# Performance work log

Hardware: AMD Instinct MI355X
Metric: run time of the kernel (lower is better)

## Reference

```python
import jax, jax.numpy as jnp
import numpy as np

# dims: batch, tokens, model dim, heads, head_dim, context len, n_blocks, ffn dim
B, L, D, H, HD, S, NB, DFF = 1, 3072, 1024, 16, 64, 512, 2, 4096
T3, H3, W3 = 12, 16, 16  # latent video grid, T3*H3*W3 == L


def _ln(x):
    # LayerNorm, elementwise_affine=False, eps=1e-6
    m = jnp.mean(x, axis=-1, keepdims=True)
    v = jnp.mean(jnp.square(x - m), axis=-1, keepdims=True)
    return (x - m) * jax.lax.rsqrt(v + 1e-6)


def _rot_half(x):
    x1, x2 = jnp.split(x, 2, axis=-1)
    return jnp.concatenate([-x2, x1], axis=-1)


def _rope3d(head_dim, t, h, w):
    d = head_dim // 6
    def band(n):
        freqs = 1.0 / 10000.0 ** (np.arange(0, 2 * d, 2, dtype=np.float32) / (2 * d))
        return np.outer(np.arange(n, dtype=np.float32), freqs)  # [n, d]
    te, he, we = band(t), band(h), band(w)
    rope = np.zeros((t, h, w, head_dim), dtype=np.float32)
    rope[:, :, :, :d] = te[:, None, None, :]
    rope[:, :, :, d:2 * d] = he[None, :, None, :]
    rope[:, :, :, 2 * d:3 * d] = we[None, None, :, :]
    return jnp.asarray(rope.reshape(t * h * w, head_dim))


def _forward(x, timestep_emb, context_emb, rope_emb, adaW, adab, sqW, skW, svW,
             soW, sob, cqW, ckW, cvW, coW, cob, f1W, f1b, f2W, f2b):
    Bv, Lv, Dv = x.shape
    hd = rope_emb.shape[-1]
    nh = Dv // hd
    scale = hd ** -0.5
    cos = jnp.cos(rope_emb)[None, None]  # [1,1,L,hd]
    sin = jnp.sin(rope_emb)[None, None]

    def heads(y):  # [B,N,D] -> [B,H,N,hd]
        return y.reshape(Bv, -1, nh, hd).transpose(0, 2, 1, 3)

    def merge(y):  # [B,H,L,hd] -> [B,L,D]
        return y.transpose(0, 2, 1, 3).reshape(Bv, Lv, Dv)

    for i in range(adaW.shape[0]):
        mods = timestep_emb @ adaW[i].T + adab[i]  # [B, 6D]
        sh_msa, sc_msa, g_msa, sh_mlp, sc_mlp, g_mlp = jnp.split(mods, 6, axis=-1)
        # --- AdaLN + self-attention with RoPE ---
        hx = _ln(x) * (1.0 + sc_msa[:, None, :]) + sh_msa[:, None, :]
        q, k, v = heads(hx @ sqW[i].T), heads(hx @ skW[i].T), heads(hx @ svW[i].T)
        q = q * cos + _rot_half(q) * sin
        k = k * cos + _rot_half(k) * sin
        a = jax.nn.softmax(jnp.einsum('bhld,bhmd->bhlm', q, k) * scale, axis=-1)
        o = merge(jnp.einsum('bhlm,bhmd->bhld', a, v))
        x = x + g_msa[:, None, :] * (o @ soW[i].T + sob[i])
        # --- cross-attention (no gate, no modulation) ---
        hx = _ln(x)
        q = heads(hx @ cqW[i].T)
        k = heads(context_emb @ ckW[i].T)
        v = heads(context_emb @ cvW[i].T)
        a = jax.nn.softmax(jnp.einsum('bhld,bhsd->bhls', q, k) * scale, axis=-1)
        o = merge(jnp.einsum('bhls,bhsd->bhld', a, v))
        x = x + (o @ coW[i].T + cob[i])
        # --- AdaLN + MLP (exact GELU) ---
        hx = _ln(x) * (1.0 + sc_mlp[:, None, :]) + sh_mlp[:, None, :]
        hx = jax.nn.gelu(hx @ f1W[i].T + f1b[i], approximate=False)
        x = x + g_mlp[:, None, :] * (hx @ f2W[i].T + f2b[i])
    return x


def setup_inputs() -> dict:
    ks = jax.random.split(jax.random.key(0), 20)
    s = 0.02
    return {
        'x': jax.random.normal(ks[0], (B, L, D), jnp.float32),
        'timestep_emb': jax.random.normal(ks[1], (B, D), jnp.float32),
        'context_emb': jax.random.normal(ks[2], (B, S, D), jnp.float32),
        'rope_emb': _rope3d(HD, T3, H3, W3),
        'adaW': jax.random.normal(ks[3], (NB, 6 * D, D), jnp.float32) * s,
        'adab': jnp.zeros((NB, 6 * D), jnp.float32),
        'sqW': jax.random.normal(ks[4], (NB, D, D), jnp.float32) * s,
        'skW': jax.random.normal(ks[5], (NB, D, D), jnp.float32) * s,
        'svW': jax.random.normal(ks[6], (NB, D, D), jnp.float32) * s,
        'soW': jax.random.normal(ks[7], (NB, D, D), jnp.float32) * s,
        'sob': jnp.zeros((NB, D), jnp.float32),
        'cqW': jax.random.normal(ks[8], (NB, D, D), jnp.float32) * s,
        'ckW': jax.random.normal(ks[9], (NB, D, D), jnp.float32) * s,
        'cvW': jax.random.normal(ks[10], (NB, D, D), jnp.float32) * s,
        'coW': jax.random.normal(ks[11], (NB, D, D), jnp.float32) * s,
        'cob': jnp.zeros((NB, D), jnp.float32),
        'f1W': jax.random.normal(ks[12], (NB, DFF, D), jnp.float32) * s,
        'f1b': jnp.zeros((NB, DFF), jnp.float32),
        'f2W': jax.random.normal(ks[13], (NB, D, DFF), jnp.float32) * s,
        'f2b': jnp.zeros((NB, D), jnp.float32),
    }


def reference(x, timestep_emb, context_emb, rope_emb, adaW, adab, sqW, skW, svW,
              soW, sob, cqW, ckW, cvW, coW, cob, f1W, f1b, f2W, f2b):
    return _forward(x, timestep_emb, context_emb, rope_emb, adaW, adab, sqW, skW,
                    svW, soW, sob, cqW, ckW, cvW, coW, cob, f1W, f1b, f2W, f2b)
```

## Files before the change

### kernel.cpp

```cpp
#include <hip/hip_runtime.h>
#include <math.h>

typedef __attribute__((ext_vector_type(8))) short bf16x8;
typedef __attribute__((ext_vector_type(4))) float f32x4;
typedef unsigned short u16;
typedef unsigned int u32;

#define DEV static __device__ __forceinline__

typedef __attribute__((address_space(3))) u32 lds_u32;
typedef const __attribute__((address_space(1))) u32 glb_u32;

DEV void gload16(const void* g, void* l){
  __builtin_amdgcn_global_load_lds((glb_u32*)g, (lds_u32*)l, 16, 0, 0);
}

DEV u16 f2bf(float f){
  u32 u = __builtin_bit_cast(u32, f);
  u32 r = (u + 0x7fffu + ((u >> 16) & 1u)) >> 16;
  return (u16)r;
}
DEV float bf2f(u16 h){
  u32 u = ((u32)h) << 16;
  return __builtin_bit_cast(float, u);
}
DEV u32 cvtpk(float a, float b){
  u32 r;
  asm("v_cvt_pk_bf16_f32 %0, %1, %2" : "=v"(r) : "v"(a), "v"(b));
  return r;
}
DEV float gelu_exact(float x){ return 0.5f*x*(1.f+erff(x*0.70710678118654752f)); }

#define QSCALE 0.18033688f

DEV void xcd_remap(int &bx, int &by){
  int gx = gridDim.x, gy = gridDim.y;
  int n = gx*gy;
  if ((n & 7) == 0){
    int id = by*gx + bx;
    int q = n >> 3;
    int sid = (id & 7)*q + (id >> 3);
    bx = sid % gx;
    by = sid / gx;
  }
}

__global__ __launch_bounds__(256) void k_copy_f32(const float* __restrict__ in, float* __restrict__ out, int n4){
  int i = blockIdx.x*256 + threadIdx.x;
  if (i < n4) ((float4*)out)[i] = ((const float4*)in)[i];
}

__global__ __launch_bounds__(256) void k_cvt_bf16(const float* __restrict__ in, u16* __restrict__ out, int n4){
  int i = blockIdx.x*256 + threadIdx.x;
  if (i < n4){
    float4 v = ((const float4*)in)[i];
    ushort4 o;
    o.x = f2bf(v.x); o.y = f2bf(v.y); o.z = f2bf(v.z); o.w = f2bf(v.w);
    ((ushort4*)out)[i] = o;
  }
}

struct CvtArgs { const float4* s[16]; ushort4* d[16]; };
__global__ __launch_bounds__(256) void k_cvt_all(CvtArgs a){
  int i = blockIdx.x*256 + threadIdx.x;
  int seg = i >> 19;
  int off = i & 0x7FFFF;
  float4 v = a.s[seg][off];
  ushort4 o;
  o.x = f2bf(v.x); o.y = f2bf(v.y); o.z = f2bf(v.z); o.w = f2bf(v.w);
  a.d[seg][off] = o;
}

__global__ __launch_bounds__(256) void k_trig(const float* __restrict__ rope,
    float2* __restrict__ ctq, float2* __restrict__ ctk){
  int i = blockIdx.x*256 + threadIdx.x;
  int d = i & 63;
  float a = rope[i];
  float c = cosf(a), s = sinf(a);
  float sg = (d < 32) ? -s : s;
  ctk[i] = make_float2(c, sg);
  ctq[i] = make_float2(c*QSCALE, sg*QSCALE);
}

__global__ __launch_bounds__(256) void k_ada(const float* __restrict__ te,
    const float* __restrict__ adaW, const float* __restrict__ adab,
    float* __restrict__ mods){
  int row = blockIdx.x*4 + (threadIdx.x>>6);
  int lane = threadIdx.x & 63;
  const float* wr = adaW + (size_t)row*1024;
  float s = 0.f;
  #pragma unroll
  for (int j=0; j<4; j++){
    int c = lane*4 + j*256;
    float4 a = *(const float4*)(te + c);
    float4 b = *(const float4*)(wr + c);
    s += a.x*b.x + a.y*b.y + a.z*b.z + a.w*b.w;
  }
  #pragma unroll
  for (int off=32; off; off>>=1) s += __shfl_down(s, off);
  if (!lane) mods[row] = s + adab[row];
}

__global__ __launch_bounds__(256) void k_ln_mod(const float* __restrict__ x,
    const float* __restrict__ sh, const float* __restrict__ sc,
    u16* __restrict__ out){
  int row = blockIdx.x, t = threadIdx.x;
  const float* xr = x + (size_t)row*1024;
  float4 v = ((const float4*)xr)[t];
  float s  = v.x+v.y+v.z+v.w;
  float sq = v.x*v.x+v.y*v.y+v.z*v.z+v.w*v.w;
  #pragma unroll
  for (int off=32; off; off>>=1){ s += __shfl_down(s,off); sq += __shfl_down(sq,off); }
  __shared__ float red[8];
  int w = t>>6, lane = t&63;
  if (!lane){ red[w] = s; red[4+w] = sq; }
  __syncthreads();
  s  = red[0]+red[1]+red[2]+red[3];
  sq = red[4]+red[5]+red[6]+red[7];
  float mean = s*(1.f/1024.f);
  float var  = sq*(1.f/1024.f) - mean*mean;
  float rst  = rsqrtf(var + 1e-6f);
  float vv[4] = {v.x, v.y, v.z, v.w};
  ushort4 o;
  u16 ob[4];
  #pragma unroll
  for (int j=0;j<4;j++){
    int col = t*4+j;
    float y = (vv[j]-mean)*rst;
    if (sh) y = y*(1.f + sc[col]) + sh[col];
    ob[j] = f2bf(y);
  }
  o.x=ob[0]; o.y=ob[1]; o.z=ob[2]; o.w=ob[3];
  *(ushort4*)(out + (size_t)row*1024 + t*4) = o;
}

__global__ __launch_bounds__(256) void k_rope(u16* __restrict__ q, u16* __restrict__ k,
    const float* __restrict__ rope){
  int idx = blockIdx.x*256 + threadIdx.x;
  int d = idx & 31;
  int h = (idx >> 5) & 15;
  int p = idx >> 9;
  const float* rr = rope + (size_t)p*64;
  float a0 = rr[d], a1 = rr[d+32];
  float c0 = cosf(a0), s0 = sinf(a0);
  float c1 = cosf(a1), s1 = sinf(a1);
  size_t o = (size_t)p*1024 + h*64 + d;
  float q0 = bf2f(q[o]), q1 = bf2f(q[o+32]);
  q[o]    = f2bf((q0*c0 - q1*s0)*QSCALE);
  q[o+32] = f2bf((q1*c1 + q0*s1)*QSCALE);
  float k0 = bf2f(k[o]), k1 = bf2f(k[o+32]);
  k[o]    = f2bf(k0*c0 - k1*s0);
  k[o+32] = f2bf(k1*c1 + k0*s1);
}

DEV void gemm_loop(const u16* __restrict__ X, const u16* __restrict__ W,
                   int bm, int bn, int ld, int lenK, u16* As, u16* Bs, f32x4 acc[4][4])
{
  int t = threadIdx.x;
  int w = t>>6, lane = t&63;
  int wr = (w>>1)*64, wc = (w&1)*64;
  int fr = lane&15, g = lane>>4;
  int arow = lane>>2, acol = (lane&3)*8;
  const u16* xp = X + (size_t)(bm + w*32 + arow)*ld + acol;
  const u16* wp = W + (size_t)(bn + w*32 + arow)*ld + acol;
  int nk = lenK >> 5;
  {
    u16* a = As + w*1024; u16* b = Bs + w*1024;
    gload16(xp, a);             gload16(xp + (size_t)16*ld, a + 512);
    gload16(wp, b);             gload16(wp + (size_t)16*ld, b + 512);
  }
  for (int kt = 0; kt < nk; ++kt){
    __syncthreads();
    int cur = kt & 1;
    if (kt + 1 < nk){
      int nb = cur ^ 1;
      int k0 = (kt+1) << 5;
      u16* a = As + nb*4096 + w*1024; u16* b = Bs + nb*4096 + w*1024;
      gload16(xp + k0, a);        gload16(xp + k0 + (size_t)16*ld, a + 512);
      gload16(wp + k0, b);        gload16(wp + k0 + (size_t)16*ld, b + 512);
    }
    const u16* ab = As + cur*4096;
    const u16* bb = Bs + cur*4096;
    bf16x8 a[4], b[4];
    #pragma unroll
    for (int i=0;i<4;i++) a[i] = *(const bf16x8*)(ab + (wr+i*16+fr)*32 + g*8);
    #pragma unroll
    for (int i=0;i<4;i++) b[i] = *(const bf16x8*)(bb + (wc+i*16+fr)*32 + g*8);
    __builtin_amdgcn_s_setprio(1);
    #pragma unroll
    for (int i=0;i<4;i++)
      #pragma unroll
      for (int j=0;j<4;j++)
        acc[i][j] = __builtin_amdgcn_mfma_f32_16x16x32_bf16(a[i], b[j], acc[i][j], 0, 0, 0);
    __builtin_amdgcn_s_setprio(0);
  }
}

template<int EPI>
__global__ __launch_bounds__(256) void k_gemm_bf16(
    const u16* __restrict__ X, const u16* __restrict__ W,
    const float* __restrict__ bias,
    u16* __restrict__ Yout,
    const float* __restrict__ resin, float* __restrict__ resout,
    const float* __restrict__ gate,
    int M, int N, int K)
{
  __shared__ __align__(16) u16 As[2*128*32];
  __shared__ __align__(16) u16 Bs[2*128*32];
  int bx = blockIdx.x, by = blockIdx.y;
  xcd_remap(bx, by);
  int bm = bx*128, bn = by*128;
  f32x4 acc[4][4] = {};
  gemm_loop(X, W, bm, bn, K, K, As, Bs, acc);
  int lane = threadIdx.x & 63, w = threadIdx.x>>6;
  int wr = (w>>1)*64, wc = (w&1)*64;
  int fr = lane&15, g = lane>>4;
  #pragma unroll
  for (int i=0;i<4;i++){
    #pragma unroll
    for (int j=0;j<4;j++){
      int col = bn + wc + j*16 + fr;
      float bv = bias ? bias[col] : 0.f;
      #pragma unroll
      for (int r=0;r<4;r++){
        int row = bm + wr + i*16 + g*4 + r;
        float y = acc[i][j][r] + bv;
        if (EPI == 1){
          Yout[(size_t)row*N + col] = f2bf(gelu_exact(y));
        } else if (EPI == 2){
          float gt = gate ? gate[col] : 1.f;
          resout[(size_t)row*N + col] = resin[(size_t)row*N + col] + gt*y;
        } else {
          Yout[(size_t)row*N + col] = f2bf(y*QSCALE);
        }
      }
    }
  }
}

__global__ __launch_bounds__(256) void k_gemm_part(
    const u16* __restrict__ X, const u16* __restrict__ W,
    float* __restrict__ pp, int M, int N, int K, int Ks)
{
  __shared__ __align__(16) u16 As[2*128*32];
  __shared__ __align__(16) u16 Bs[2*128*32];
  int bx = blockIdx.x, by = blockIdx.y;
  xcd_remap(bx, by);
  int s = blockIdx.z;
  int bm = bx*128, bn = by*128;
  f32x4 acc[4][4] = {};
  gemm_loop(X + (size_t)s*Ks, W + (size_t)s*Ks, bm, bn, K, Ks, As, Bs, acc);
  float* out = pp + (size_t)s*M*N;
  int lane = threadIdx.x & 63, w = threadIdx.x>>6;
  int wr = (w>>1)*64, wc = (w&1)*64;
  int fr = lane&15, g = lane>>4;
  #pragma unroll
  for (int i=0;i<4;i++)
    #pragma unroll
    for (int j=0;j<4;j++){
      int col = bn + wc + j*16 + fr;
      #pragma unroll
      for (int r=0;r<4;r++){
        int row = bm + wr + i*16 + g*4 + r;
        out[(size_t)row*N + col] = acc[i][j][r];
      }
    }
}

template<int EPI>
__global__ __launch_bounds__(256) void k_reduce(
    const float* __restrict__ pp, int S, const float* __restrict__ bias,
    const float* __restrict__ resin, float* __restrict__ resout,
    const float* __restrict__ gate, u16* __restrict__ Ybf,
    int MN, int N)
{
  int idx = blockIdx.x*256 + threadIdx.x;
  int base = idx*4;
  if (base >= MN) return;
  float4 s4 = *(const float4*)(pp + base);
  for (int s=1; s<S; ++s){
    float4 t4 = *(const float4*)(pp + (size_t)s*MN + base);
    s4.x += t4.x; s4.y += t4.y; s4.z += t4.z; s4.w += t4.w;
  }
  int col = base & (N-1);
  float b0=0,b1=0,b2=0,b3=0;
  if (bias){ b0=bias[col]; b1=bias[col+1]; b2=bias[col+2]; b3=bias[col+3]; }
  if (EPI == 2){
    float g0=1,g1=1,g2=1,g3=1;
    if (gate){ g0=gate[col]; g1=gate[col+1]; g2=gate[col+2]; g3=gate[col+3]; }
    float4 rv = *(const float4*)(resin + base);
    float4 o;
    o.x = rv.x + g0*(s4.x+b0);
    o.y = rv.y + g1*(s4.y+b1);
    o.z = rv.z + g2*(s4.z+b2);
    o.w = rv.w + g3*(s4.w+b3);
    *(float4*)(resout + base) = o;
  } else {
    ushort4 o;
    o.x = f2bf((s4.x+b0)*QSCALE);
    o.y = f2bf((s4.y+b1)*QSCALE);
    o.z = f2bf((s4.z+b2)*QSCALE);
    o.w = f2bf((s4.w+b3)*QSCALE);
    *(ushort4*)(Ybf + base) = o;
  }
}

template<int MOD>
__global__ __launch_bounds__(256) void k_reduce_ln(
    const float* __restrict__ pp, int S, const float* __restrict__ bias,
    const float* __restrict__ resin, float* __restrict__ resout,
    const float* __restrict__ gate,
    const float* __restrict__ sh, const float* __restrict__ sc,
    u16* __restrict__ hx)
{
  int row = blockIdx.x, t = threadIdx.x;
  size_t base = (size_t)row*1024 + t*4;
  const size_t MN = (size_t)3072*1024;
  float4 s4 = *(const float4*)(pp + base);
  for (int s=1; s<S; ++s){
    float4 t4 = *(const float4*)(pp + (size_t)s*MN + base);
    s4.x += t4.x; s4.y += t4.y; s4.z += t4.z; s4.w += t4.w;
  }
  int col = t*4;
  float b0=0,b1=0,b2=0,b3=0;
  if (bias){ b0=bias[col]; b1=bias[col+1]; b2=bias[col+2]; b3=bias[col+3]; }
  float g0=1,g1=1,g2=1,g3=1;
  if (gate){ g0=gate[col]; g1=gate[col+1]; g2=gate[col+2]; g3=gate[col+3]; }
  float4 rv = *(const float4*)(resin + base);
  float y[4];
  y[0] = rv.x + g0*(s4.x+b0);
  y[1] = rv.y + g1*(s4.y+b1);
  y[2] = rv.z + g2*(s4.z+b2);
  y[3] = rv.w + g3*(s4.w+b3);
  float4 ov; ov.x=y[0]; ov.y=y[1]; ov.z=y[2]; ov.w=y[3];
  *(float4*)(resout + base) = ov;
  float s  = y[0]+y[1]+y[2]+y[3];
  float sq = y[0]*y[0]+y[1]*y[1]+y[2]*y[2]+y[3]*y[3];
  #pragma unroll
  for (int off=32; off; off>>=1){ s += __shfl_down(s,off); sq += __shfl_down(sq,off); }
  __shared__ float red[8];
  int w = t>>6, lane = t&63;
  if (!lane){ red[w] = s; red[4+w] = sq; }
  __syncthreads();
  s  = red[0]+red[1]+red[2]+red[3];
  sq = red[4]+red[5]+red[6]+red[7];
  float mean = s*(1.f/1024.f);
  float var  = sq*(1.f/1024.f) - mean*mean;
  float rst  = rsqrtf(var + 1e-6f);
  ushort4 o;
  u16 ob[4];
  #pragma unroll
  for (int j=0;j<4;j++){
    float yy = (y[j]-mean)*rst;
    if (MOD) yy = yy*(1.f + sc[col+j]) + sh[col+j];
    ob[j] = f2bf(yy);
  }
  o.x=ob[0]; o.y=ob[1]; o.z=ob[2]; o.w=ob[3];
  *(ushort4*)(hx + base) = o;
}

template<int MODE>
__global__ __launch_bounds__(256) void k_qkv(
    const u16* __restrict__ X,
    const u16* __restrict__ W0, const u16* __restrict__ W1, const u16* __restrict__ W2,
    u16* __restrict__ Y0, u16* __restrict__ Y1, u16* __restrict__ VT,
    const float2* __restrict__ ctq, const float2* __restrict__ ctk,
    int M, int ldvt)
{
  __shared__ __align__(16) u16 As[2*128*32];
  __shared__ __align__(16) u16 Bs[2*128*32];
  int bx = blockIdx.x, by = blockIdx.y;
  xcd_remap(bx, by);
  int bm = bx*128, bn = by*128;
  int sel = bn >> 10;
  int bnl = bn & 1023;
  const u16* W = (sel==0 ? W0 : (sel==1 ? W1 : W2));
  f32x4 acc[4][4] = {};
  gemm_loop(X, W, bm, bnl, 1024, 1024, As, Bs, acc);
  int lane = threadIdx.x & 63, w = threadIdx.x>>6;
  int wr = (w>>1)*64, wc = (w&1)*64;
  int fr = lane&15, g = lane>>4;
  if (sel < 2){
    u16* Y = (sel==0) ? Y0 : Y1;
    const float2* ct = (sel==0) ? ctq : ctk;
    #pragma unroll
    for (int i=0;i<4;i++)
      #pragma unroll
      for (int j=0;j<4;j++){
        int col = bnl + wc + j*16 + fr;
        int d = j*16 + fr;
        #pragma unroll
        for (int r=0;r<4;r++){
          int row = bm + wr + i*16 + g*4 + r;
          float2 cs = ct[row*64 + d];
          float yv = acc[i][j][r]*cs.x + acc[i][j^2][r]*cs.y;
          Y[(size_t)row*1024 + col] = f2bf(yv);
        }
      }
  } else {
    #pragma unroll
    for (int i=0;i<4;i++)
      #pragma unroll
      for (int j=0;j<4;j++){
        int col = bnl + wc + j*16 + fr;
        int row0 = bm + wr + i*16 + g*4;
        uint2 pk;
        pk.x = cvtpk(acc[i][j][0], acc[i][j][1]);
        pk.y = cvtpk(acc[i][j][2], acc[i][j][3]);
        *(uint2*)(VT + (size_t)col*ldvt + row0) = pk;
      }
  }
}

__global__ __launch_bounds__(256) void k_kv64(
    const u16* __restrict__ X,
    const u16* __restrict__ Wk, const u16* __restrict__ Wv,
    u16* __restrict__ Kout, u16* __restrict__ VTout, int ldvt)
{
  __shared__ __align__(16) u16 As[2*64*32];
  __shared__ __align__(16) u16 Bs[2*64*32];
  int bx = blockIdx.x, by = blockIdx.y;
  xcd_remap(bx, by);
  int bm = bx*64;
  int sel = by >> 4;
  int bnl = (by & 15)*64;
  const u16* W = sel ? Wv : Wk;
  int t = threadIdx.x, w = t>>6, lane = t&63;
  int wr = (w>>1)*32, wc = (w&1)*32;
  int fr = lane&15, g = lane>>4;
  f32x4 acc[2][2] = {};
  int arow = lane>>2, acol = (lane&3)*8;
  const u16* xp = X + (size_t)(bm + w*16 + arow)*1024 + acol;
  const u16* wp = W + (size_t)(bnl + w*16 + arow)*1024 + acol;
  {
    gload16(xp, As + w*512);
    gload16(wp, Bs + w*512);
  }
  for (int kt = 0; kt < 32; ++kt){
    __syncthreads();
    int cur = kt & 1;
    if (kt + 1 < 32){
      int nb = cur ^ 1;
      int k0 = (kt+1) << 5;
      gload16(xp + k0, As + nb*2048 + w*512);
      gload16(wp + k0, Bs + nb*2048 + w*512);
    }
    const u16* ab = As + cur*2048;
    const u16* bb = Bs + cur*2048;
    bf16x8 a[2], b[2];
    #pragma unroll
    for (int i=0;i<2;i++) a[i] = *(const bf16x8*)(ab + (wr+i*16+fr)*32 + g*8);
    #pragma unroll
    for (int i=0;i<2;i++) b[i] = *(const bf16x8*)(bb + (wc+i*16+fr)*32 + g*8);
    __builtin_amdgcn_s_setprio(1);
    #pragma unroll
    for (int i=0;i<2;i++)
      #pragma unroll
      for (int j=0;j<2;j++)
        acc[i][j] = __builtin_amdgcn_mfma_f32_16x16x32_bf16(a[i], b[j], acc[i][j], 0, 0, 0);
    __builtin_amdgcn_s_setprio(0);
  }
  #pragma unroll
  for (int i=0;i<2;i++)
    #pragma unroll
    for (int j=0;j<2;j++){
      int col = bnl + wc + j*16 + fr;
      if (sel == 0){
        #pragma unroll
        for (int r=0;r<4;r++){
          int row = bm + wr + i*16 + g*4 + r;
          Kout[(size_t)row*1024 + col] = f2bf(acc[i][j][r]);
        }
      } else {
        int row0 = bm + wr + i*16 + g*4;
        uint2 pk;
        pk.x = cvtpk(acc[i][j][0], acc[i][j][1]);
        pk.y = cvtpk(acc[i][j][2], acc[i][j][3]);
        *(uint2*)(VTout + (size_t)col*ldvt + row0) = pk;
      }
    }
}

template<int EPI>
__global__ __launch_bounds__(256) void k_gemm_f32(
    const u16* __restrict__ X, const float* __restrict__ W,
    const float* __restrict__ bias,
    u16* __restrict__ Yout,
    const float* __restrict__ resin, float* __restrict__ resout,
    const float* __restrict__ gate,
    int M, int N, int K)
{
  __shared__ __align__(16) u16 As[128][32];
  __shared__ __align__(16) u16 Bs[128][40];
  int bx = blockIdx.x, by = blockIdx.y;
  xcd_remap(bx, by);
  int bm = bx*128, bn = by*128;
  int t = threadIdx.x;
  int w = t>>6, lane = t&63;
  int wr = (w>>1)*64, wc = (w&1)*64;
  int fr = lane&15, g = lane>>4;
  f32x4 acc[4][4] = {};
  int arow = lane>>2, acol = (lane&3)*8;
  int srow = t>>2, scol = (t&3)*8;
  for (int k0=0; k0<K; k0+=32){
    #pragma unroll
    for (int inst=0; inst<2; ++inst){
      int r = w*32 + inst*16 + arow;
      gload16(X + (size_t)(bm+r)*K + k0 + acol, &As[w*32+inst*16][0]);
    }
    #pragma unroll
    for (int it=0; it<2; ++it){
      const float* wp = W + (size_t)(bn+srow+it*64)*K + k0 + scol;
      float4 f0 = *(const float4*)(wp);
      float4 f1 = *(const float4*)(wp+4);
      uint4 bw;
      bw.x = (u32)f2bf(f0.x) | ((u32)f2bf(f0.y)<<16);
      bw.y = (u32)f2bf(f0.z) | ((u32)f2bf(f0.w)<<16);
      bw.z = (u32)f2bf(f1.x) | ((u32)f2bf(f1.y)<<16);
      bw.w = (u32)f2bf(f1.z) | ((u32)f2bf(f1.w)<<16);
      *(uint4*)&Bs[srow+it*64][scol] = bw;
    }
    __syncthreads();
    bf16x8 a[4], b[4];
    #pragma unroll
    for (int i=0;i<4;i++) a[i] = *(const bf16x8*)&As[wr+i*16+fr][g*8];
    #pragma unroll
    for (int i=0;i<4;i++) b[i] = *(const bf16x8*)&Bs[wc+i*16+fr][g*8];
    #pragma unroll
    for (int i=0;i<4;i++)
      #pragma unroll
      for (int j=0;j<4;j++)
        acc[i][j] = __builtin_amdgcn_mfma_f32_16x16x32_bf16(a[i], b[j], acc[i][j], 0, 0, 0);
    __syncthreads();
  }
  #pragma unroll
  for (int i=0;i<4;i++){
    #pragma unroll
    for (int j=0;j<4;j++){
      int col = bn + wc + j*16 + fr;
      float bv = bias ? bias[col] : 0.f;
      #pragma unroll
      for (int r=0;r<4;r++){
        int row = bm + wr + i*16 + g*4 + r;
        float y = acc[i][j][r] + bv;
        if (EPI == 0){
          Yout[(size_t)row*N + col] = f2bf(y);
        } else if (EPI == 1){
          Yout[(size_t)row*N + col] = f2bf(gelu_exact(y));
        } else if (EPI == 2){
          float gt = gate ? gate[col] : 1.f;
          resout[(size_t)row*N + col] = resin[(size_t)row*N + col] + gt*y;
        } else if (EPI == 3){
          Yout[(size_t)col*M + row] = f2bf(y);
        } else {
          Yout[(size_t)row*N + col] = f2bf(y*QSCALE);
        }
      }
    }
  }
}

__global__ __launch_bounds__(256) void k_flash(
    const u16* __restrict__ Q, const u16* __restrict__ Kb, const u16* __restrict__ VT,
    u16* __restrict__ O, int Lkv)
{
  __shared__ __align__(16) u16 Ks[2*64*64];
  __shared__ __align__(16) u16 Vs[2*64*64];
  __shared__ __align__(16) u16 Ps[4][16][72];
  int bx = blockIdx.x, by = blockIdx.y;
  xcd_remap(bx, by);
  int h = by;
  int q0 = bx*64;
  int t = threadIdx.x, w = t>>6, lane = t&63;
  int fr = lane&15, g = lane>>4;
  const u16* qrow = Q + (size_t)(q0 + w*16 + fr)*1024 + h*64;
  bf16x8 aq0 = *(const bf16x8*)(qrow + g*8);
  bf16x8 aq1 = *(const bf16x8*)(qrow + 32 + g*8);
  f32x4 accO[4] = {};
  float l = 0.f;
  int slot = lane & 7, rop = lane >> 3;
  const u16* kbase = Kb + (size_t)h*64;
  const u16* vbase = VT + (size_t)h*64*Lkv;
  int nt = Lkv >> 6;
  auto stage = [&](int tt){
    int buf = tt & 1;
    int k0 = tt << 6;
    #pragma unroll
    for (int inst=0; inst<2; ++inst){
      int row = w*16 + inst*8 + rop;
      int ss = slot ^ (row & 7);
      gload16(kbase + (size_t)(k0+row)*1024 + ss*8, Ks + buf*4096 + row*64);
      gload16(vbase + (size_t)row*Lkv + k0 + ss*8, Vs + buf*4096 + row*64);
    }
  };
  stage(0);
  bf16x8 vp0[4], vp1[4];
  for (int tt=0; tt<nt; ++tt){
    __syncthreads();
    int cur = tt & 1;
    const u16* kc = Ks + cur*4096;
    const u16* vc = Vs + cur*4096;
    bf16x8 vn0[4], vn1[4];
    #pragma unroll
    for (int nd=0; nd<4; nd++){
      int rowV = nd*16 + fr;
      vn0[nd] = *(const bf16x8*)(vc + rowV*64 + ((g  ) ^ (rowV&7))*8);
      vn1[nd] = *(const bf16x8*)(vc + rowV*64 + ((4+g) ^ (rowV&7))*8);
    }
    bf16x8 ap0, ap1;
    if (tt > 0){
      ap0 = *(const bf16x8*)&Ps[w][fr][g*8];
      ap1 = *(const bf16x8*)&Ps[w][fr][32 + g*8];
    }
    if (tt+1 < nt) stage(tt+1);
    f32x4 st[4] = {};
    __builtin_amdgcn_s_setprio(1);
    #pragma unroll
    for (int kb=0;kb<4;kb++){
      int rowK = kb*16 + fr;
      bf16x8 b0 = *(const bf16x8*)(kc + rowK*64 + ((g  ) ^ (rowK&7))*8);
      bf16x8 b1 = *(const bf16x8*)(kc + rowK*64 + ((4+g) ^ (rowK&7))*8);
      st[kb] = __builtin_amdgcn_mfma_f32_16x16x32_bf16(b0, aq0, st[kb], 0,0,0);
      st[kb] = __builtin_amdgcn_mfma_f32_16x16x32_bf16(b1, aq1, st[kb], 0,0,0);
    }
    if (tt > 0){
      #pragma unroll
      for (int nd=0; nd<4; nd++){
        accO[nd] = __builtin_amdgcn_mfma_f32_16x16x32_bf16(ap0, vp0[nd], accO[nd], 0,0,0);
        accO[nd] = __builtin_amdgcn_mfma_f32_16x16x32_bf16(ap1, vp1[nd], accO[nd], 0,0,0);
      }
    }
    __builtin_amdgcn_s_setprio(0);
    float ts = 0.f;
    u32 pk[8];
    #pragma unroll
    for (int kb=0;kb<4;kb++){
      float p0 = exp2f(st[kb][0]);
      float p1 = exp2f(st[kb][1]);
      float p2 = exp2f(st[kb][2]);
      float p3 = exp2f(st[kb][3]);
      ts += (p0+p1)+(p2+p3);
      pk[kb*2]   = cvtpk(p0,p1);
      pk[kb*2+1] = cvtpk(p2,p3);
    }
    ts += __shfl_xor(ts, 16);
    ts += __shfl_xor(ts, 32);
    l += ts;
    #pragma unroll
    for (int kb=0;kb<4;kb++){
      uint2 pv; pv.x = pk[kb*2]; pv.y = pk[kb*2+1];
      *(uint2*)&Ps[w][fr][kb*16 + g*4] = pv;
    }
    #pragma unroll
    for (int nd=0; nd<4; nd++){ vp0[nd] = vn0[nd]; vp1[nd] = vn1[nd]; }
  }
  {
    bf16x8 ap0 = *(const bf16x8*)&Ps[w][fr][g*8];
    bf16x8 ap1 = *(const bf16x8*)&Ps[w][fr][32 + g*8];
    #pragma unroll
    for (int nd=0; nd<4; nd++){
      accO[nd] = __builtin_amdgcn_mfma_f32_16x16x32_bf16(ap0, vp0[nd], accO[nd], 0,0,0);
      accO[nd] = __builtin_amdgcn_mfma_f32_16x16x32_bf16(ap1, vp1[nd], accO[nd], 0,0,0);
    }
  }
  float rl = 1.f / l;
  #pragma unroll
  for (int r=0;r<4;r++){
    float rlq = __shfl(rl, g*4+r);
    int row = q0 + w*16 + g*4 + r;
    #pragma unroll
    for (int nd=0; nd<4; nd++)
      O[(size_t)row*1024 + h*64 + nd*16 + fr] = f2bf(accO[nd][r] * rlq);
  }
}

extern "C" void kernel_launch(void* const* d_in, const int* in_sizes, int n_in,
                              void* d_out, int out_size, void* d_ws, size_t ws_size,
                              hipStream_t stream){
  const float* x_in = (const float*)d_in[0];
  const float* te   = (const float*)d_in[1];
  const float* ctx  = (const float*)d_in[2];
  const float* rope = (const float*)d_in[3];
  const float* adaW = (const float*)d_in[4];
  const float* adab = (const float*)d_in[5];
  const float* sqW  = (const float*)d_in[6];
  const float* skW  = (const float*)d_in[7];
  const float* svW  = (const float*)d_in[8];
  const float* soW  = (const float*)d_in[9];
  const float* sob  = (const float*)d_in[10];
  const float* cqW  = (const float*)d_in[11];
  const float* ckW  = (const float*)d_in[12];
  const float* cvW  = (const float*)d_in[13];
  const float* coW  = (const float*)d_in[14];
  const float* cob  = (const float*)d_in[15];
  const float* f1W  = (const float*)d_in[16];
  const float* f1b  = (const float*)d_in[17];
  const float* f2W  = (const float*)d_in[18];
  const float* f2b  = (const float*)d_in[19];
  float* x = (float*)d_out;

  char* p = (char*)d_ws;
  size_t used = 0;
  auto alloc = [&](size_t bytes){
    void* r = (void*)(p + used);
    used += (bytes + 255) & ~(size_t)255;
    return r;
  };
  u16* hx   = (u16*)alloc((size_t)3072*1024*2);
  u16* qb   = (u16*)alloc((size_t)3072*1024*2);
  u16* kb   = (u16*)alloc((size_t)3072*1024*2);
  u16* vt   = (u16*)alloc((size_t)1024*3072*2);
  u16* ob   = (u16*)alloc((size_t)3072*1024*2);
  u16* mid  = (u16*)alloc((size_t)3072*4096*2);
  u16* ctxb = (u16*)alloc((size_t)512*1024*2);
  float* mods = (float*)alloc((size_t)2*6144*4);
  float2* ctq = (float2*)alloc((size_t)3072*64*8);
  float2* ctk = (float2*)alloc((size_t)3072*64*8);
  size_t base_used = used;
  const size_t NW_SMALL = (size_t)2*1024*1024;
  const size_t NW_BIG   = (size_t)2*4096*1024;
  size_t wbytes = (8*NW_SMALL + 2*NW_BIG)*2;
  bool pre = (base_used + wbytes + 4096) <= ws_size;

  u16 *sqWb=nullptr,*skWb=nullptr,*svWb=nullptr,*soWb=nullptr,
      *cqWb=nullptr,*ckWb=nullptr,*cvWb=nullptr,*coWb=nullptr,
      *f1Wb=nullptr,*f2Wb=nullptr;
  if (pre){
    sqWb=(u16*)alloc(NW_SMALL*2); skWb=(u16*)alloc(NW_SMALL*2);
    svWb=(u16*)alloc(NW_SMALL*2); soWb=(u16*)alloc(NW_SMALL*2);
    cqWb=(u16*)alloc(NW_SMALL*2); ckWb=(u16*)alloc(NW_SMALL*2);
    cvWb=(u16*)alloc(NW_SMALL*2); coWb=(u16*)alloc(NW_SMALL*2);
    f1Wb=(u16*)alloc(NW_BIG*2);   f2Wb=(u16*)alloc(NW_BIG*2);
  }
  const size_t PPN = (size_t)4*3072*1024;
  float* pp = nullptr;
  bool splitok = pre && (used + PPN*4 + 4096) <= ws_size;
  if (splitok) pp = (float*)alloc(PPN*4);
  const int MN = 3072*1024;

  if (pre){
    CvtArgs ca;
    const float* smallW[8] = {sqW,skW,svW,soW,cqW,ckW,cvW,coW};
    u16* smallD[8] = {sqWb,skWb,svWb,soWb,cqWb,ckWb,cvWb,coWb};
    for (int s=0; s<8; ++s){ ca.s[s] = (const float4*)smallW[s]; ca.d[s] = (ushort4*)smallD[s]; }
    for (int qd=0; qd<4; ++qd){
      ca.s[8+qd]  = (const float4*)f1W + (size_t)qd*524288;
      ca.d[8+qd]  = (ushort4*)f1Wb + (size_t)qd*524288;
      ca.s[12+qd] = (const float4*)f2W + (size_t)qd*524288;
      ca.d[12+qd] = (ushort4*)f2Wb + (size_t)qd*524288;
    }
    k_cvt_all<<<32768, 256, 0, stream>>>(ca);
  }
  k_cvt_bf16<<<512, 256, 0, stream>>>(ctx, ctxb, 131072);
  k_ada<<<3072, 256, 0, stream>>>(te, adaW, adab, mods);
  k_trig<<<768, 256, 0, stream>>>(rope, ctq, ctk);
  if (!splitok) k_copy_f32<<<3072, 256, 0, stream>>>(x_in, x, 786432);

  for (int i=0; i<2; ++i){
    const float* mi  = mods + (size_t)i*6144;
    const float* mi2 = mods + 6144;
    size_t wo = (size_t)i*1024*1024;
    size_t wof = (size_t)i*4096*1024;
    if (i == 0 || !splitok)
      k_ln_mod<<<3072,256,0,stream>>>(i==0 ? x_in : x, mi+0, mi+1024, hx);
    if (pre){
      k_qkv<0><<<dim3(24,24),256,0,stream>>>(hx, sqWb+wo, skWb+wo, svWb+wo, qb, kb, vt, ctq, ctk, 3072, 3072);
    } else {
      k_gemm_f32<0><<<dim3(24,8),256,0,stream>>>(hx, sqW+wo, nullptr, qb, nullptr,nullptr,nullptr, 3072,1024,1024);
      k_gemm_f32<0><<<dim3(24,8),256,0,stream>>>(hx, skW+wo, nullptr, kb, nullptr,nullptr,nullptr, 3072,1024,1024);
      k_gemm_f32<3><<<dim3(24,8),256,0,stream>>>(hx, svW+wo, nullptr, vt, nullptr,nullptr,nullptr, 3072,1024,1024);
      k_rope<<<6144,256,0,stream>>>(qb, kb, rope);
    }
    k_flash<<<dim3(48,16),256,0,stream>>>(qb, kb, vt, ob, 3072);
    if (splitok){
      k_gemm_part<<<dim3(24,8,2),256,0,stream>>>(ob, soWb+wo, pp, 3072,1024,1024,512);
      k_reduce_ln<0><<<3072,256,0,stream>>>(pp, 2, sob+(size_t)i*1024,
          (i==0 ? x_in : (const float*)x), x, mi+2048, nullptr, nullptr, hx);
    } else if (pre){
      k_gemm_bf16<2><<<dim3(24,8),256,0,stream>>>(ob, soWb+wo, sob+(size_t)i*1024, nullptr, x, x, mi+2048, 3072,1024,1024);
      k_ln_mod<<<3072,256,0,stream>>>(x, nullptr, nullptr, hx);
    } else {
      k_gemm_f32<2><<<dim3(24,8),256,0,stream>>>(ob, soW+wo, sob+(size_t)i*1024, nullptr, x, x, mi+2048, 3072,1024,1024);
      k_ln_mod<<<3072,256,0,stream>>>(x, nullptr, nullptr, hx);
    }
    if (splitok){
      k_gemm_part<<<dim3(24,8,2),256,0,stream>>>(hx, cqWb+wo, pp, 3072,1024,1024,512);
      k_reduce<4><<<3072,256,0,stream>>>(pp, 2, nullptr, nullptr, nullptr, nullptr, qb, MN, 1024);
      k_kv64<<<dim3(8,32),256,0,stream>>>(ctxb, ckWb+wo, cvWb+wo, kb, vt, 512);
    } else if (pre){
      k_gemm_bf16<4><<<dim3(24,8),256,0,stream>>>(hx, cqWb+wo, nullptr, qb, nullptr,nullptr,nullptr, 3072,1024,1024);
      k_kv64<<<dim3(8,32),256,0,stream>>>(ctxb, ckWb+wo, cvWb+wo, kb, vt, 512);
    } else {
      k_gemm_f32<4><<<dim3(24,8),256,0,stream>>>(hx, cqW+wo, nullptr, qb, nullptr,nullptr,nullptr, 3072,1024,1024);
      k_gemm_f32<0><<<dim3(4,8),256,0,stream>>>(ctxb, ckW+wo, nullptr, kb, nullptr,nullptr,nullptr, 512,1024,1024);
      k_gemm_f32<3><<<dim3(4,8),256,0,stream>>>(ctxb, cvW+wo, nullptr, vt, nullptr,nullptr,nullptr, 512,1024,1024);
    }
    k_flash<<<dim3(48,16),256,0,stream>>>(qb, kb, vt, ob, 512);
    if (splitok){
      k_gemm_part<<<dim3(24,8,2),256,0,stream>>>(ob, coWb+wo, pp, 3072,1024,1024,512);
      k_reduce_ln<1><<<3072,256,0,stream>>>(pp, 2, cob+(size_t)i*1024, x, x, nullptr, mi+3072, mi+4096, hx);
    } else if (pre){
      k_gemm_bf16<2><<<dim3(24,8),256,0,stream>>>(ob, coWb+wo, cob+(size_t)i*1024, nullptr, x, x, nullptr, 3072,1024,1024);
      k_ln_mod<<<3072,256,0,stream>>>(x, mi+3072, mi+4096, hx);
    } else {
      k_gemm_f32<2><<<dim3(24,8),256,0,stream>>>(ob, coW+wo, cob+(size_t)i*1024, nullptr, x, x, nullptr, 3072,1024,1024);
      k_ln_mod<<<3072,256,0,stream>>>(x, mi+3072, mi+4096, hx);
    }
    if (pre){
      k_gemm_bf16<1><<<dim3(24,32),256,0,stream>>>(hx, f1Wb+wof, f1b+(size_t)i*4096, mid, nullptr,nullptr,nullptr, 3072,4096,1024);
    } else {
      k_gemm_f32<1><<<dim3(24,32),256,0,stream>>>(hx, f1W+wof, f1b+(size_t)i*4096, mid, nullptr,nullptr,nullptr, 3072,4096,1024);
    }
    if (splitok){
      k_gemm_part<<<dim3(24,8,4),256,0,stream>>>(mid, f2Wb+wof, pp, 3072,1024,4096,1024);
      if (i == 0)
        k_reduce_ln<1><<<3072,256,0,stream>>>(pp, 4, f2b, x, x, mi+5120, mi2+0, mi2+1024, hx);
      else
        k_reduce<2><<<3072,256,0,stream>>>(pp, 4, f2b+1024, x, x, mi+5120, nullptr, MN, 1024);
    } else if (pre){
      k_gemm_bf16<2><<<dim3(24,8),256,0,stream>>>(mid, f2Wb+wof, f2b+(size_t)i*1024, nullptr, x, x, mi+5120, 3072,1024,4096);
    } else {
      k_gemm_f32<2><<<dim3(24,8),256,0,stream>>>(mid, f2W+wof, f2b+(size_t)i*1024, nullptr, x, x, mi+5120, 3072,1024,4096);
    }
  }
}
```

Baseline: 788.8 us.

## Un-skew flash attention PV pipeline and XOR-swizzle the P tile in LDS

The flash kernel previously deferred each tile's P·V MFMAs to the next iteration and carried V fragments in registers across iterations. Now P·V runs in the same iteration, with V read directly from LDS. The P scratch buffer changes from a padded [16][72] layout to an unpadded 64-wide layout with an XOR swizzle to avoid bank conflicts. This lowers register pressure and LDS footprint but drops the cross-iteration overlap of the softmax exp work with the previous tile's MFMAs.

```diff
diff --git a/kernel.cpp b/kernel.cpp
--- a/kernel.cpp
+++ b/kernel.cpp
@@ -566,7 +566,7 @@
 {
   __shared__ __align__(16) u16 Ks[2*64*64];
   __shared__ __align__(16) u16 Vs[2*64*64];
-  __shared__ __align__(16) u16 Ps[4][16][72];
+  __shared__ __align__(16) u16 Ps[4*16*64];
   int bx = blockIdx.x, by = blockIdx.y;
   xcd_remap(bx, by);
   int h = by;
@@ -582,37 +582,33 @@
   const u16* kbase = Kb + (size_t)h*64;
   const u16* vbase = VT + (size_t)h*64*Lkv;
   int nt = Lkv >> 6;
-  auto stage = [&](int tt){
-    int buf = tt & 1;
-    int k0 = tt << 6;
+  u16* pbase = Ps + w*1024 + fr*64;
+  int pswz = (fr & 7) << 3;
+  {
     #pragma unroll
     for (int inst=0; inst<2; ++inst){
       int row = w*16 + inst*8 + rop;
       int ss = slot ^ (row & 7);
-      gload16(kbase + (size_t)(k0+row)*1024 + ss*8, Ks + buf*4096 + row*64);
-      gload16(vbase + (size_t)row*Lkv + k0 + ss*8, Vs + buf*4096 + row*64);
-    }
-  };
-  stage(0);
-  bf16x8 vp0[4], vp1[4];
+      gload16(kbase + (size_t)row*1024 + ss*8, Ks + (w*16+inst*8)*64);
+      gload16(vbase + (size_t)row*Lkv + ss*8, Vs + (w*16+inst*8)*64);
+    }
+  }
   for (int tt=0; tt<nt; ++tt){
     __syncthreads();
     int cur = tt & 1;
+    if (tt+1 < nt){
+      int nb = cur ^ 1;
+      int k0 = (tt+1) << 6;
+      #pragma unroll
+      for (int inst=0; inst<2; ++inst){
+        int row = w*16 + inst*8 + rop;
+        int ss = slot ^ (row & 7);
+        gload16(kbase + (size_t)(k0+row)*1024 + ss*8, Ks + nb*4096 + (w*16+inst*8)*64);
+        gload16(vbase + (size_t)row*Lkv + k0 + ss*8, Vs + nb*4096 + (w*16+inst*8)*64);
+      }
+    }
     const u16* kc = Ks + cur*4096;
     const u16* vc = Vs + cur*4096;
-    bf16x8 vn0[4], vn1[4];
-    #pragma unroll
-    for (int nd=0; nd<4; nd++){
-      int rowV = nd*16 + fr;
-      vn0[nd] = *(const bf16x8*)(vc + rowV*64 + ((g  ) ^ (rowV&7))*8);
-      vn1[nd] = *(const bf16x8*)(vc + rowV*64 + ((4+g) ^ (rowV&7))*8);
-    }
-    bf16x8 ap0, ap1;
-    if (tt > 0){
-      ap0 = *(const bf16x8*)&Ps[w][fr][g*8];
-      ap1 = *(const bf16x8*)&Ps[w][fr][32 + g*8];
-    }
-    if (tt+1 < nt) stage(tt+1);
     f32x4 st[4] = {};
     __builtin_amdgcn_s_setprio(1);
     #pragma unroll
@@ -622,13 +618,6 @@
       bf16x8 b1 = *(const bf16x8*)(kc + rowK*64 + ((4+g) ^ (rowK&7))*8);
       st[kb] = __builtin_amdgcn_mfma_f32_16x16x32_bf16(b0, aq0, st[kb], 0,0,0);
       st[kb] = __builtin_amdgcn_mfma_f32_16x16x32_bf16(b1, aq1, st[kb], 0,0,0);
-    }
-    if (tt > 0){
-      #pragma unroll
-      for (int nd=0; nd<4; nd++){
-        accO[nd] = __builtin_amdgcn_mfma_f32_16x16x32_bf16(ap0, vp0[nd], accO[nd], 0,0,0);
-        accO[nd] = __builtin_amdgcn_mfma_f32_16x16x32_bf16(ap1, vp1[nd], accO[nd], 0,0,0);
-      }
     }
     __builtin_amdgcn_s_setprio(0);
     float ts = 0.f;
@@ -649,19 +638,20 @@
     #pragma unroll
     for (int kb=0;kb<4;kb++){
       uint2 pv; pv.x = pk[kb*2]; pv.y = pk[kb*2+1];
-      *(uint2*)&Ps[w][fr][kb*16 + g*4] = pv;
-    }
-    #pragma unroll
-    for (int nd=0; nd<4; nd++){ vp0[nd] = vn0[nd]; vp1[nd] = vn1[nd]; }
-  }
-  {
-    bf16x8 ap0 = *(const bf16x8*)&Ps[w][fr][g*8];
-    bf16x8 ap1 = *(const bf16x8*)&Ps[w][fr][32 + g*8];
+      *(uint2*)(pbase + ((kb*16 + g*4) ^ pswz)) = pv;
+    }
+    bf16x8 ap0 = *(const bf16x8*)(pbase + ((g*8) ^ pswz));
+    bf16x8 ap1 = *(const bf16x8*)(pbase + ((32 + g*8) ^ pswz));
+    __builtin_amdgcn_s_setprio(1);
     #pragma unroll
     for (int nd=0; nd<4; nd++){
-      accO[nd] = __builtin_amdgcn_mfma_f32_16x16x32_bf16(ap0, vp0[nd], accO[nd], 0,0,0);
-      accO[nd] = __builtin_amdgcn_mfma_f32_16x16x32_bf16(ap1, vp1[nd], accO[nd], 0,0,0);
-    }
+      int rowV = nd*16 + fr;
+      bf16x8 b0 = *(const bf16x8*)(vc + rowV*64 + ((g  ) ^ (rowV&7))*8);
+      bf16x8 b1 = *(const bf16x8*)(vc + rowV*64 + ((4+g) ^ (rowV&7))*8);
+      accO[nd] = __builtin_amdgcn_mfma_f32_16x16x32_bf16(ap0, b0, accO[nd], 0,0,0);
+      accO[nd] = __builtin_amdgcn_mfma_f32_16x16x32_bf16(ap1, b1, accO[nd], 0,0,0);
+    }
+    __builtin_amdgcn_s_setprio(0);
   }
   float rl = 1.f / l;
   #pragma unroll
```

Result: faster. 764.5 us (median of 2 runs) (-3.1%).
